# Kernel tuning notes

Measured on AMD Instinct MI355X. Metric: run time of the kernel, lower is better.

## Reference

```python
import jax, jax.numpy as jnp
import numpy as np

GRID_DIM = 7
NQUERIES = 100
C = 256

def setup_inputs() -> dict:
    key = jax.random.key(0)
    k1, k2 = jax.random.split(key)
    images = jax.random.normal(k1, (4, 224, 224, C), dtype=jnp.float32)
    # learned query weight (orthogonal init in original; random normal is fine as a stand-in)
    queries = jax.random.normal(k2, (NQUERIES, C), dtype=jnp.float32)
    return {"images": images, "queries": queries}

def _positions(g):
    lin = jnp.linspace(0.0, 1.0, g + 1)[:-1].astype(jnp.float32)
    # positions[i*g + j] = (lin[i], lin[j]) -> (h_frac, w_frac), row-major over the grid
    return jnp.stack(jnp.meshgrid(lin, lin, indexing="ij"), axis=-1).reshape(g * g, 2)

def reference(images, queries):
    g = GRID_DIM
    B, H, W, Cc = images.shape
    h, w = H // g, W // g
    # batch-extract all grid regions at once: [B, g*g, h*w, C]
    regions = images.reshape(B, g, h, g, w, Cc)
    regions = regions.transpose(0, 1, 3, 2, 4, 5).reshape(B, g * g, h * w, Cc)
    # keras Attention (dot, no scale): softmax(Q K^T) V, queries shared across batch/regions
    scores = jnp.einsum("qc,bnsc->bnqs", queries, regions)  # [B, g*g, nq, h*w]
    attn = jax.nn.softmax(scores, axis=-1)
    out = jnp.einsum("bnqs,bnsc->bnqc", attn, regions)  # [B, g*g, nq, C]
    return out, _positions(g)
```

## Files before the change

### kernel.cpp

```cpp
#include <hip/hip_runtime.h>
#include <stdint.h>

typedef short short8 __attribute__((ext_vector_type(8)));
typedef __fp16 fp16x8 __attribute__((ext_vector_type(8)));
typedef float f32x16 __attribute__((ext_vector_type(16)));
typedef unsigned int uint;

#define NREG 49
#define NQ   100
#define CC   256
#define OUT_POS_OFF 5017600
#define PO_PER (NQ*CC)
#define QF_BYTES 65536
#define MFMA_BF16 __builtin_amdgcn_mfma_f32_32x32x16_bf16
#define MFMA_F16  __builtin_amdgcn_mfma_f32_32x32x16_f16

union U4H8 { uint4 u; fp16x8 h; short8 s; };

#define LBAR() do { \
    asm volatile("s_waitcnt lgkmcnt(0)" ::: "memory"); \
    __builtin_amdgcn_s_barrier(); \
} while (0)

__device__ __forceinline__ uint pkrtz(float a, float b){
    auto v = __builtin_amdgcn_cvt_pkrtz(a, b);
    return __builtin_bit_cast(uint, v);
}
__device__ __forceinline__ uint16_t f2bf_rne(float x){
    uint u = __float_as_uint(x);
    u += 0x7fffu + ((u >> 16) & 1u);
    return (uint16_t)(u >> 16);
}
__device__ __forceinline__ float bf2f(uint16_t b){
    return __uint_as_float(((uint)b) << 16);
}

__global__ __launch_bounds__(512) void qfrag_kernel(const float* __restrict__ Qg,
                                                    uint4* __restrict__ qf){
    int gid  = blockIdx.x * 512 + threadIdx.x;
    int lane = gid & 63;
    int frag = gid >> 6;
    int k    = frag & 15;
    int qt   = frag >> 4;
    int q    = qt * 32 + (lane & 31);
    int c0   = k * 16 + (lane >> 5) * 8;
    float v[8];
#pragma unroll
    for (int j = 0; j < 8; ++j) v[j] = (q < NQ) ? Qg[q * CC + c0 + j] : 0.f;
    qf[gid] = make_uint4(pkrtz(v[0], v[1]), pkrtz(v[2], v[3]),
                         pkrtz(v[4], v[5]), pkrtz(v[6], v[7]));
}

__global__ __launch_bounds__(512, 2) void attn_kernel(
        const float* __restrict__ img, const uint4* __restrict__ qf,
        float* __restrict__ out, float* __restrict__ po,
        float* __restrict__ pl, int split)
{
    __shared__ __align__(16) unsigned char smem[65536];
    unsigned char* sRT = smem;
    unsigned char* sU  = smem + 32768;

    const int tid = threadIdx.x;
    const int seg = blockIdx.x % split;
    const int bn  = blockIdx.x / split;
    const int rr  = bn % NREG;
    const int bb  = bn / NREG;
    const int gh  = rr / 7, gw = rr % 7;

    if (bn == 0 && seg == 0 && tid < NREG){
        out[OUT_POS_OFF + 2 * tid]     = (float)((tid / 7) / 7.0);
        out[OUT_POS_OFF + 2 * tid + 1] = (float)((tid % 7) / 7.0);
    }

    const int lane = tid & 63, w = tid >> 6;
    const int l31  = lane & 31;
    const int st = w & 1, qt = w >> 1;
    const int mp = w & 1, cq = w >> 1;

    const int sloc = tid >> 3;
    const int ct   = tid & 7;
    const int stw  = sloc >> 5;
    const int s31  = sloc & 31;
    const int ksw  = sloc >> 4;
    const int lhw  = (sloc >> 3) & 1;
    const int jw   = sloc & 7;
    const int rtwbase = ((ksw * 8 + ct) * 64 + lhw * 32) * 16 + jw * 2;
    const int afwbase = (stw * 16 + ct * 2) * 1024 + s31 * 16;

    const float* rbase = img + ((size_t)(bb * 224 + gh * 32) * 224 + gw * 32) * CC;

    uint4 qr[16];
#pragma unroll
    for (int k = 0; k < 16; ++k) qr[k] = qf[(qt * 16 + k) * 64 + lane];

    f32x16 acc00, acc01, acc10, acc11;
#pragma unroll
    for (int i = 0; i < 16; ++i){ acc00[i]=0.f; acc01[i]=0.f; acc10[i]=0.f; acc11[i]=0.f; }
    float lp = 0.f;
    const int qq = qt * 32 + l31;

    const int nch = 16 / split;
    const int ch0 = seg * nch, ch1 = ch0 + nch;

    float4 rb[8], rb2[8];
    {
        int p = ch0 * 64 + sloc;
        const float* gp = rbase + ((p >> 5) * 224 + (p & 31)) * CC + ct * 32;
#pragma unroll
        for (int j = 0; j < 8; ++j) rb[j] = *(const float4*)(gp + j * 4);
    }

    for (int ch = ch0; ch < ch1; ++ch){
#pragma unroll
        for (int r = 0; r < 4; ++r){
            uint4 o = make_uint4(pkrtz(rb[2*r].x,   rb[2*r].y),
                                 pkrtz(rb[2*r].z,   rb[2*r].w),
                                 pkrtz(rb[2*r+1].x, rb[2*r+1].y),
                                 pkrtz(rb[2*r+1].z, rb[2*r+1].w));
            *(uint4*)(sU + afwbase + ((r >> 1) * 1024) + ((r & 1) * 512)) = o;
        }
#pragma unroll
        for (int i = 0; i < 32; ++i){
            const float* fp = (const float*)rb;
            uint u = __float_as_uint(fp[i]);
            *(uint16_t*)(sRT + rtwbase + ((i ^ ct) << 4)) = (uint16_t)(u >> 16);
        }

        if (ch + 1 < ch1){
            int p = (ch + 1) * 64 + sloc;
            const float* gp = rbase + ((p >> 5) * 224 + (p & 31)) * CC + ct * 32;
#pragma unroll
            for (int j = 0; j < 8; ++j) rb2[j] = *(const float4*)(gp + j * 4);
        }
        LBAR();

        f32x16 a1;
#pragma unroll
        for (int i = 0; i < 16; ++i) a1[i] = 0.f;
#pragma unroll
        for (int k = 0; k < 16; ++k){
            U4H8 af; af.u = *(const uint4*)(sU + ((st * 16 + k) * 64 + lane) * 16);
            U4H8 bq; bq.u = qr[k];
            a1 = MFMA_F16(af.h, bq.h, a1, 0, 0, 0);
        }
        LBAR();

#pragma unroll
        for (int g2 = 0; g2 < 4; ++g2){
            uint16_t e[4];
#pragma unroll
            for (int r2 = 0; r2 < 4; ++r2){
                float sc = a1[g2 * 4 + r2];
                float pv = exp2f(sc * 1.4426950408889634f - 57.70780163555852f);
                e[r2] = f2bf_rne(pv);
                lp += bf2f(e[r2]);
            }
            int kst = st * 2 + (g2 >> 1);
            int boff = ((kst * 4 + qt) * 64 + (g2 & 1) * 32 + l31) * 16 + (lane >> 5) * 8;
            *(uint2*)(sU + boff) = make_uint2((uint)e[0] | ((uint)e[1] << 16),
                                              (uint)e[2] | ((uint)e[3] << 16));
        }
        LBAR();

#pragma unroll
        for (int ks = 0; ks < 4; ++ks){
            U4H8 A0, A1, B0, B1;
            A0.u = *(const uint4*)(sU  + ((ks * 4 + mp * 2    ) * 64 + lane) * 16);
            A1.u = *(const uint4*)(sU  + ((ks * 4 + mp * 2 + 1) * 64 + lane) * 16);
            B0.u = *(const uint4*)(sRT + ((ks * 8 + cq * 2    ) * 64 + (lane ^ (cq * 2    ))) * 16);
            B1.u = *(const uint4*)(sRT + ((ks * 8 + cq * 2 + 1) * 64 + (lane ^ (cq * 2 + 1))) * 16);
            acc00 = MFMA_BF16(A0.s, B0.s, acc00, 0, 0, 0);
            acc01 = MFMA_BF16(A0.s, B1.s, acc01, 0, 0, 0);
            acc10 = MFMA_BF16(A1.s, B0.s, acc10, 0, 0, 0);
            acc11 = MFMA_BF16(A1.s, B1.s, acc11, 0, 0, 0);
        }
        LBAR();

        if (ch + 1 < ch1){
#pragma unroll
            for (int j = 0; j < 8; ++j) rb[j] = rb2[j];
        }
    }

    float* sL = (float*)sU;
    if (tid < 128) sL[tid] = 0.f;
    __syncthreads();
    atomicAdd(&sL[qq], lp);
    __syncthreads();

    const int c0 = cq * 64 + l31;
    if (split == 1){
        float* ob = out + (size_t)bn * PO_PER;
#pragma unroll
        for (int r = 0; r < 16; ++r){
            int row = (r & 3) + 8 * (r >> 2) + 4 * (lane >> 5);
            int q0 = mp * 64 + row, q1 = q0 + 32;
            if (q0 < NQ){
                float inv = 1.0f / sL[q0];
                ob[q0 * CC + c0]      = acc00[r] * inv;
                ob[q0 * CC + c0 + 32] = acc01[r] * inv;
            }
            if (q1 < NQ){
                float inv = 1.0f / sL[q1];
                ob[q1 * CC + c0]      = acc10[r] * inv;
                ob[q1 * CC + c0 + 32] = acc11[r] * inv;
            }
        }
    } else {
        float* ob = po + ((size_t)bn * split + seg) * PO_PER;
#pragma unroll
        for (int r = 0; r < 16; ++r){
            int row = (r & 3) + 8 * (r >> 2) + 4 * (lane >> 5);
            int q0 = mp * 64 + row, q1 = q0 + 32;
            if (q0 < NQ){
                ob[q0 * CC + c0]      = acc00[r];
                ob[q0 * CC + c0 + 32] = acc01[r];
            }
            if (q1 < NQ){
                ob[q1 * CC + c0]      = acc10[r];
                ob[q1 * CC + c0 + 32] = acc11[r];
            }
        }
        if (tid < 128) pl[((size_t)bn * split + seg) * 128 + tid] = sL[tid];
    }
}

__global__ __launch_bounds__(512) void reduce_kernel(
        const float* __restrict__ po, const float* __restrict__ pl,
        float* __restrict__ out, int split)
{
    __shared__ float sInv[64];
    const int bn = blockIdx.x >> 1, hf = blockIdx.x & 1, tid = threadIdx.x;
    if (tid < 50){
        int q = hf * 50 + tid;
        float s = 0.f;
        for (int g = 0; g < split; ++g)
            s += pl[((size_t)bn * split + g) * 128 + q];
        sInv[tid] = 1.0f / s;
    }
    __syncthreads();
    const float* base = po + (size_t)bn * split * PO_PER;
    float* ob = out + (size_t)bn * PO_PER;
#pragma unroll 1
    for (int i = 0; i < 25; ++i){
        int idx = hf * 12800 + i * 512 + tid;
        float s = 0.f;
        for (int g = 0; g < split; ++g) s += base[g * PO_PER + idx];
        ob[idx] = s * sInv[(idx >> 8) - hf * 50];
    }
}

extern "C" void kernel_launch(void* const* d_in, const int* in_sizes, int n_in,
                              void* d_out, int out_size, void* d_ws, size_t ws_size,
                              hipStream_t stream){
    const float* img = (const float*)d_in[0];
    const float* Qg  = (const float*)d_in[1];
    float* out = (float*)d_out;

    uint4* qf = (uint4*)d_ws;
    qfrag_kernel<<<8, 512, 0, stream>>>(Qg, qf);

    int split = 1;
    const size_t per_seg = (size_t)196 * (PO_PER + 128) * sizeof(float);
    if (ws_size >= QF_BYTES + 4 * per_seg) split = 4;

    float *po = nullptr, *pl = nullptr;
    if (split > 1){
        po = (float*)((char*)d_ws + QF_BYTES);
        pl = po + (size_t)196 * split * PO_PER;
    }

    attn_kernel<<<196 * split, 512, 0, stream>>>(img, qf, out, po, pl, split);
    if (split > 1)
        reduce_kernel<<<392, 512, 0, stream>>>(po, pl, out, split);
}
```

Measured before the change: 359.5 us.

## Load PV B-operand directly from global and double-buffer the P tile

Drops the transposed bf16 copy of the region in shared memory. Each wave now reads its own 32-channel column slice of the region straight from global memory (a strided gather that should hit cache) and packs it into registers as the B operand of the PV matmul. The PV work is repartitioned so each wave owns 32 channels across all 128 query rows. A double-buffered P tile lets two of the four barriers per chunk be removed. The trade-off is extra scalar-strided global loads per chunk and more register pressure, in exchange for fewer LDS writes and fewer syncs.

Result: slower. 399.1 us (+11.0%).

```diff
diff --git a/kernel.cpp b/kernel.cpp
--- a/kernel.cpp
+++ b/kernel.cpp
@@ -57,8 +57,7 @@
         float* __restrict__ pl, int split)
 {
     __shared__ __align__(16) unsigned char smem[65536];
-    unsigned char* sRT = smem;
-    unsigned char* sU  = smem + 32768;
+    unsigned char* sAf = smem;
 
     const int tid = threadIdx.x;
     const int seg = blockIdx.x % split;
@@ -74,35 +73,33 @@
 
     const int lane = tid & 63, w = tid >> 6;
     const int l31  = lane & 31;
+    const int h2   = lane >> 5;
     const int st = w & 1, qt = w >> 1;
-    const int mp = w & 1, cq = w >> 1;
 
     const int sloc = tid >> 3;
     const int ct   = tid & 7;
     const int stw  = sloc >> 5;
     const int s31  = sloc & 31;
-    const int ksw  = sloc >> 4;
-    const int lhw  = (sloc >> 3) & 1;
-    const int jw   = sloc & 7;
-    const int rtwbase = ((ksw * 8 + ct) * 64 + lhw * 32) * 16 + jw * 2;
     const int afwbase = (stw * 16 + ct * 2) * 1024 + s31 * 16;
 
+    const int c2 = w * 32 + l31;
+
     const float* rbase = img + ((size_t)(bb * 224 + gh * 32) * 224 + gw * 32) * CC;
 
     uint4 qr[16];
 #pragma unroll
     for (int k = 0; k < 16; ++k) qr[k] = qf[(qt * 16 + k) * 64 + lane];
 
-    f32x16 acc00, acc01, acc10, acc11;
-#pragma unroll
-    for (int i = 0; i < 16; ++i){ acc00[i]=0.f; acc01[i]=0.f; acc10[i]=0.f; acc11[i]=0.f; }
+    f32x16 acc0, acc1, acc2, acc3;
+#pragma unroll
+    for (int i = 0; i < 16; ++i){ acc0[i]=0.f; acc1[i]=0.f; acc2[i]=0.f; acc3[i]=0.f; }
     float lp = 0.f;
     const int qq = qt * 32 + l31;
 
     const int nch = 16 / split;
     const int ch0 = seg * nch, ch1 = ch0 + nch;
 
-    float4 rb[8], rb2[8];
+    float4 rb[8];
     {
         int p = ch0 * 64 + sloc;
         const float* gp = rbase + ((p >> 5) * 224 + (p & 31)) * CC + ct * 32;
@@ -111,27 +108,35 @@
     }
 
     for (int ch = ch0; ch < ch1; ++ch){
+        unsigned char* sP = smem + 32768 + ((ch & 1) << 14);
+
 #pragma unroll
         for (int r = 0; r < 4; ++r){
             uint4 o = make_uint4(pkrtz(rb[2*r].x,   rb[2*r].y),
                                  pkrtz(rb[2*r].z,   rb[2*r].w),
                                  pkrtz(rb[2*r+1].x, rb[2*r+1].y),
                                  pkrtz(rb[2*r+1].z, rb[2*r+1].w));
-            *(uint4*)(sU + afwbase + ((r >> 1) * 1024) + ((r & 1) * 512)) = o;
-        }
-#pragma unroll
-        for (int i = 0; i < 32; ++i){
-            const float* fp = (const float*)rb;
-            uint u = __float_as_uint(fp[i]);
-            *(uint16_t*)(sRT + rtwbase + ((i ^ ct) << 4)) = (uint16_t)(u >> 16);
+            *(uint4*)(sAf + afwbase + ((r >> 1) * 1024) + ((r & 1) * 512)) = o;
         }
 
         if (ch + 1 < ch1){
             int p = (ch + 1) * 64 + sloc;
             const float* gp = rbase + ((p >> 5) * 224 + (p & 31)) * CC + ct * 32;
 #pragma unroll
-            for (int j = 0; j < 8; ++j) rb2[j] = *(const float4*)(gp + j * 4);
-        }
+            for (int j = 0; j < 8; ++j) rb[j] = *(const float4*)(gp + j * 4);
+        }
+
+        float s2[32];
+#pragma unroll
+        for (int cc = 0; cc < 4; ++cc){
+#pragma unroll
+            for (int j = 0; j < 8; ++j){
+                int sp = cc * 16 + h2 * 8 + j;
+                int pp = ch * 64 + sp;
+                s2[cc * 8 + j] = rbase[((size_t)(pp >> 5) * 224 + (pp & 31)) * CC + c2];
+            }
+        }
+
         LBAR();
 
         f32x16 a1;
@@ -139,11 +144,10 @@
         for (int i = 0; i < 16; ++i) a1[i] = 0.f;
 #pragma unroll
         for (int k = 0; k < 16; ++k){
-            U4H8 af; af.u = *(const uint4*)(sU + ((st * 16 + k) * 64 + lane) * 16);
+            U4H8 af; af.u = *(const uint4*)(sAf + ((st * 16 + k) * 64 + lane) * 16);
             U4H8 bq; bq.u = qr[k];
             a1 = MFMA_F16(af.h, bq.h, a1, 0, 0, 0);
         }
-        LBAR();
 
 #pragma unroll
         for (int g2 = 0; g2 < 4; ++g2){
@@ -156,70 +160,68 @@
                 lp += bf2f(e[r2]);
             }
             int kst = st * 2 + (g2 >> 1);
-            int boff = ((kst * 4 + qt) * 64 + (g2 & 1) * 32 + l31) * 16 + (lane >> 5) * 8;
-            *(uint2*)(sU + boff) = make_uint2((uint)e[0] | ((uint)e[1] << 16),
+            int boff = ((kst * 4 + qt) * 64 + (g2 & 1) * 32 + l31) * 16 + h2 * 8;
+            *(uint2*)(sP + boff) = make_uint2((uint)e[0] | ((uint)e[1] << 16),
                                               (uint)e[2] | ((uint)e[3] << 16));
         }
+
+        uint4 rf[4];
+#pragma unroll
+        for (int cc = 0; cc < 4; ++cc){
+            uint pk0 = (__float_as_uint(s2[cc*8+0]) >> 16) | (__float_as_uint(s2[cc*8+1]) & 0xffff0000u);
+            uint pk1 = (__float_as_uint(s2[cc*8+2]) >> 16) | (__float_as_uint(s2[cc*8+3]) & 0xffff0000u);
+            uint pk2 = (__float_as_uint(s2[cc*8+4]) >> 16) | (__float_as_uint(s2[cc*8+5]) & 0xffff0000u);
+            uint pk3 = (__float_as_uint(s2[cc*8+6]) >> 16) | (__float_as_uint(s2[cc*8+7]) & 0xffff0000u);
+            rf[cc] = make_uint4(pk0, pk1, pk2, pk3);
+        }
+
         LBAR();
 
 #pragma unroll
         for (int ks = 0; ks < 4; ++ks){
-            U4H8 A0, A1, B0, B1;
-            A0.u = *(const uint4*)(sU  + ((ks * 4 + mp * 2    ) * 64 + lane) * 16);
-            A1.u = *(const uint4*)(sU  + ((ks * 4 + mp * 2 + 1) * 64 + lane) * 16);
-            B0.u = *(const uint4*)(sRT + ((ks * 8 + cq * 2    ) * 64 + (lane ^ (cq * 2    ))) * 16);
-            B1.u = *(const uint4*)(sRT + ((ks * 8 + cq * 2 + 1) * 64 + (lane ^ (cq * 2 + 1))) * 16);
-            acc00 = MFMA_BF16(A0.s, B0.s, acc00, 0, 0, 0);
-            acc01 = MFMA_BF16(A0.s, B1.s, acc01, 0, 0, 0);
-            acc10 = MFMA_BF16(A1.s, B0.s, acc10, 0, 0, 0);
-            acc11 = MFMA_BF16(A1.s, B1.s, acc11, 0, 0, 0);
-        }
-        LBAR();
-
-        if (ch + 1 < ch1){
-#pragma unroll
-            for (int j = 0; j < 8; ++j) rb[j] = rb2[j];
-        }
-    }
-
-    float* sL = (float*)sU;
+            U4H8 B; B.u = rf[ks];
+            U4H8 A0, A1, A2, A3;
+            A0.u = *(const uint4*)(sP + ((ks * 4 + 0) * 64 + lane) * 16);
+            A1.u = *(const uint4*)(sP + ((ks * 4 + 1) * 64 + lane) * 16);
+            A2.u = *(const uint4*)(sP + ((ks * 4 + 2) * 64 + lane) * 16);
+            A3.u = *(const uint4*)(sP + ((ks * 4 + 3) * 64 + lane) * 16);
+            acc0 = MFMA_BF16(A0.s, B.s, acc0, 0, 0, 0);
+            acc1 = MFMA_BF16(A1.s, B.s, acc1, 0, 0, 0);
+            acc2 = MFMA_BF16(A2.s, B.s, acc2, 0, 0, 0);
+            acc3 = MFMA_BF16(A3.s, B.s, acc3, 0, 0, 0);
+        }
+    }
+
+    __syncthreads();
+
+    float* sL = (float*)(smem + 32768);
     if (tid < 128) sL[tid] = 0.f;
     __syncthreads();
     atomicAdd(&sL[qq], lp);
     __syncthreads();
 
-    const int c0 = cq * 64 + l31;
+    const int c0 = w * 32 + l31;
     if (split == 1){
         float* ob = out + (size_t)bn * PO_PER;
 #pragma unroll
         for (int r = 0; r < 16; ++r){
-            int row = (r & 3) + 8 * (r >> 2) + 4 * (lane >> 5);
-            int q0 = mp * 64 + row, q1 = q0 + 32;
-            if (q0 < NQ){
-                float inv = 1.0f / sL[q0];
-                ob[q0 * CC + c0]      = acc00[r] * inv;
-                ob[q0 * CC + c0 + 32] = acc01[r] * inv;
-            }
-            if (q1 < NQ){
-                float inv = 1.0f / sL[q1];
-                ob[q1 * CC + c0]      = acc10[r] * inv;
-                ob[q1 * CC + c0 + 32] = acc11[r] * inv;
-            }
+            int row = (r & 3) + 8 * (r >> 2) + 4 * h2;
+            ob[(row     ) * CC + c0] = acc0[r] / sL[row     ];
+            ob[(row + 32) * CC + c0] = acc1[r] / sL[row + 32];
+            ob[(row + 64) * CC + c0] = acc2[r] / sL[row + 64];
+            if (row + 96 < NQ)
+                ob[(row + 96) * CC + c0] = acc3[r] / sL[row + 96];
         }
     } else {
         float* ob = po + ((size_t)bn * split + seg) * PO_PER;
 #pragma unroll
         for (int r = 0; r < 16; ++r){
-            int row = (r & 3) + 8 * (r >> 2) + 4 * (lane >> 5);
-            int q0 = mp * 64 + row, q1 = q0 + 32;
-            if (q0 < NQ){
-                ob[q0 * CC + c0]      = acc00[r];
-                ob[q0 * CC + c0 + 32] = acc01[r];
-            }
-            if (q1 < NQ){
-                ob[q1 * CC + c0]      = acc10[r];
-                ob[q1 * CC + c0 + 32] = acc11[r];
-            }
+            int row = (r & 3) + 8 * (r >> 2) + 4 * h2;
+            ob[(row     ) * CC + c0] = acc0[r];
+            ob[(row + 32) * CC + c0] = acc1[r];
+            ob[(row + 64) * CC + c0] = acc2[r];
+            if (row + 96 < NQ)
+                ob[(row + 96) * CC + c0] = acc3[r];
         }
         if (tid < 128) pl[((size_t)bn * split + seg) * 128 + tid] = sL[tid];
     }
```

## Remap global loads to lane-contiguous channels and swizzle LDS fragment writes

Applied to the files above, without the earlier changes.

Global loads of the region tile are reassigned so each wave reads one pixel row with lanes covering contiguous 4-channel chunks, instead of each thread reading 32 consecutive channels. This aims to fully coalesce global reads. The LDS layouts for the f16 key fragments and the bf16 transposed value tile are rewritten to match, with an XOR swizzle on the key fragment buffer applied to both the writes and the MFMA operand reads to avoid bank conflicts. The cost is more complex index arithmetic and narrower LDS stores (uint2 instead of uint4).

Result: no change. 354.1 us (-1.5%).

```diff
diff --git a/kernel.cpp b/kernel.cpp
--- a/kernel.cpp
+++ b/kernel.cpp
@@ -77,15 +77,11 @@
     const int st = w & 1, qt = w >> 1;
     const int mp = w & 1, cq = w >> 1;
 
-    const int sloc = tid >> 3;
-    const int ct   = tid & 7;
-    const int stw  = sloc >> 5;
-    const int s31  = sloc & 31;
-    const int ksw  = sloc >> 4;
-    const int lhw  = (sloc >> 3) & 1;
-    const int jw   = sloc & 7;
-    const int rtwbase = ((ksw * 8 + ct) * 64 + lhw * 32) * 16 + jw * 2;
-    const int afwbase = (stw * 16 + ct * 2) * 1024 + s31 * 16;
+    const int kA    = lane >> 2;
+    const int aInP  = 32 * ((lane >> 1) & 1) * 16 + (lane & 1) * 8;
+    const int aSwz  = (kA & 7) << 4;
+    const int cb    = lane >> 3;
+    const int c31b  = 4 * (lane & 7);
 
     const float* rbase = img + ((size_t)(bb * 224 + gh * 32) * 224 + gw * 32) * CC;
 
@@ -104,33 +100,36 @@
 
     float4 rb[8], rb2[8];
     {
-        int p = ch0 * 64 + sloc;
-        const float* gp = rbase + ((p >> 5) * 224 + (p & 31)) * CC + ct * 32;
-#pragma unroll
-        for (int j = 0; j < 8; ++j) rb[j] = *(const float4*)(gp + j * 4);
+#pragma unroll
+        for (int j = 0; j < 8; ++j){
+            int p = ch0 * 64 + j * 8 + w;
+            rb[j] = *(const float4*)(rbase + ((p >> 5) * 224 + (p & 31)) * CC + 4 * lane);
+        }
     }
 
     for (int ch = ch0; ch < ch1; ++ch){
 #pragma unroll
-        for (int r = 0; r < 4; ++r){
-            uint4 o = make_uint4(pkrtz(rb[2*r].x,   rb[2*r].y),
-                                 pkrtz(rb[2*r].z,   rb[2*r].w),
-                                 pkrtz(rb[2*r+1].x, rb[2*r+1].y),
-                                 pkrtz(rb[2*r+1].z, rb[2*r+1].w));
-            *(uint4*)(sU + afwbase + ((r >> 1) * 1024) + ((r & 1) * 512)) = o;
-        }
-#pragma unroll
-        for (int i = 0; i < 32; ++i){
-            const float* fp = (const float*)rb;
-            uint u = __float_as_uint(fp[i]);
-            *(uint16_t*)(sRT + rtwbase + ((i ^ ct) << 4)) = (uint16_t)(u >> 16);
+        for (int j = 0; j < 8; ++j){
+            int pl_ = j * 8 + w;
+            int frag  = (pl_ >> 5) * 16 + kA;
+            int inner = (((pl_ & 31) * 16 + aInP)) ^ aSwz;
+            uint2 val = make_uint2(pkrtz(rb[j].x, rb[j].y), pkrtz(rb[j].z, rb[j].w));
+            *(uint2*)(sU + frag * 1024 + inner) = val;
+            const float* fv = (const float*)&rb[j];
+            int fbase = ((j >> 1) * 8 + cb) * 1024 + (j & 1) * 512 + w * 2;
+#pragma unroll
+            for (int cc = 0; cc < 4; ++cc){
+                uint u = __float_as_uint(fv[cc]);
+                *(uint16_t*)(sRT + fbase + (((c31b + cc) ^ cb) << 4)) = (uint16_t)(u >> 16);
+            }
         }
 
         if (ch + 1 < ch1){
-            int p = (ch + 1) * 64 + sloc;
-            const float* gp = rbase + ((p >> 5) * 224 + (p & 31)) * CC + ct * 32;
-#pragma unroll
-            for (int j = 0; j < 8; ++j) rb2[j] = *(const float4*)(gp + j * 4);
+#pragma unroll
+            for (int j = 0; j < 8; ++j){
+                int p = (ch + 1) * 64 + j * 8 + w;
+                rb2[j] = *(const float4*)(rbase + ((p >> 5) * 224 + (p & 31)) * CC + 4 * lane);
+            }
         }
         LBAR();
 
@@ -139,7 +138,7 @@
         for (int i = 0; i < 16; ++i) a1[i] = 0.f;
 #pragma unroll
         for (int k = 0; k < 16; ++k){
-            U4H8 af; af.u = *(const uint4*)(sU + ((st * 16 + k) * 64 + lane) * 16);
+            U4H8 af; af.u = *(const uint4*)(sU + (st * 16 + k) * 1024 + ((lane * 16) ^ ((k & 7) << 4)));
             U4H8 bq; bq.u = qr[k];
             a1 = MFMA_F16(af.h, bq.h, a1, 0, 0, 0);
         }
```
